# Kernel optimization log

Measured on AMD Instinct MI355X. Metric: run time of the kernel, lower is better.

The kernel has to match this reference:

```python
import jax, jax.numpy as jnp
import numpy as np
import math

N, S, C, K, V = 32, 4096, 1, 512, 128
TARGET_SCALE = 0.06  # normalize_scale == embedding_scale when normalize=True


def setup_inputs() -> dict:
    key = jax.random.key(0)
    k1, k2 = jax.random.split(key)
    x0 = jax.random.normal(k1, (N, S, C, V), dtype=jnp.float32)
    emb = jax.random.normal(k2, (C, K, V), dtype=jnp.float32) * TARGET_SCALE
    # after_update(): renormalize each code vector to norm = embedding_scale*sqrt(V)
    tn = TARGET_SCALE * math.sqrt(V)
    emb = emb * (tn / jnp.linalg.norm(emb, axis=2, keepdims=True))
    return {"x0": x0, "embedding0": emb}


def _vq_forward(x0, embedding0):
    tn = TARGET_SCALE * math.sqrt(V)
    # normalize inputs and codebook to the same norm (normalize=True path)
    x = tn * x0 / jnp.linalg.norm(x0, axis=3, keepdims=True)              # (N,S,C,V)
    emb = tn * embedding0 / jnp.linalg.norm(embedding0, axis=2, keepdims=True)  # (C,K,V)

    xf = x.reshape(N * S, C, V)
    x2 = jnp.sum(xf * xf, axis=2)                     # (NS, C)
    e2 = jnp.sum(emb * emb, axis=2)                   # (C, K)
    dots = jnp.einsum('ncv,ckv->nck', xf, emb)        # (NS, C, K)
    d2 = x2[:, :, None] + e2[None, :, :] - 2.0 * dots
    index = jnp.argmin(d2, axis=2)                    # (NS, C) int

    # entropy of code usage: histc over n_classes, normalized by len(index)=NS
    hist = jnp.zeros((K,), jnp.float32).at[index.reshape(-1)].add(1.0)
    prob = hist / float(N * S)
    entropy = -jnp.sum(jnp.where(hist > 0, prob * jnp.log(jnp.where(hist > 0, prob, 1.0)), 0.0))

    # gather selected code vectors per channel
    output = emb[jnp.arange(C)[None, :], index]       # (NS, C, V)
    output = output.reshape(x.shape)                  # (N,S,C,V)

    sg = jax.lax.stop_gradient
    out0 = sg(output - x) + x                                              # straight-through
    out1 = jnp.sum((sg(x) - output) ** 2, axis=3)                          # codebook loss (N,S,C)
    out2 = jnp.sum((x - sg(output)) ** 2, axis=3) + jnp.sum((x - x0) ** 2, axis=3)  # commitment + norm penalty
    return out0, out1, out2, entropy


def reference(x0, embedding0):
    return _vq_forward(x0, embedding0)
```

## Files before the change

kernel.cpp:

```cpp
#include <hip/hip_runtime.h>
#include <math.h>

#define VDIM   128
#define KCODES 512
#define NROWS  (32 * 4096)
#define TILE_ROWS 512
#define NBLK (NROWS / TILE_ROWS)
#define TN 0.67882250993908565f

typedef __attribute__((ext_vector_type(8))) short bf16x8;
typedef __attribute__((ext_vector_type(4))) float f32x4;

__device__ __forceinline__ unsigned short f2bf(float f) {
    unsigned u = __float_as_uint(f);
    unsigned r = u + 0x7FFFu + ((u >> 16) & 1u);
    return (unsigned short)(r >> 16);
}

__device__ __forceinline__ bf16x8 pack8(f32x4 a, f32x4 b) {
    bf16x8 v;
    v[0] = (short)f2bf(a[0]); v[1] = (short)f2bf(a[1]);
    v[2] = (short)f2bf(a[2]); v[3] = (short)f2bf(a[3]);
    v[4] = (short)f2bf(b[0]); v[5] = (short)f2bf(b[1]);
    v[6] = (short)f2bf(b[2]); v[7] = (short)f2bf(b[3]);
    return v;
}

__global__ __launch_bounds__(1024, 4) void vq_fused(
        const float* __restrict__ x0,
        const float* __restrict__ emb0,
        unsigned short* __restrict__ hist_part,
        float* __restrict__ out0,
        float* __restrict__ out1,
        float* __restrict__ out2) {
    __shared__ uint4 sB[8192];
    __shared__ float sscale[KCODES];
    __shared__ int   shist[KCODES];
    __shared__ int   sbesti[TILE_ROWS];
    __shared__ float sdot[TILE_ROWS];
    __shared__ float sn0[TILE_ROWS];

    int t = threadIdx.x;
    int w = t >> 6;
    int l = t & 63;
    int n15 = l & 15;
    int q = l >> 4;

    int rowbase = blockIdx.x * TILE_ROWS + (w << 5);
    f32x4 ax[2][4][2];
    #pragma unroll
    for (int s = 0; s < 2; ++s) {
        const float* xrow = x0 + (size_t)(rowbase + (s << 4) + n15) * VDIM + (q << 3);
        #pragma unroll
        for (int kc = 0; kc < 4; ++kc) {
            const f32x4* xp = (const f32x4*)(xrow + (kc << 5));
            ax[s][kc][0] = __builtin_nontemporal_load(xp);
            ax[s][kc][1] = __builtin_nontemporal_load(xp + 1);
        }
    }

    if (t < KCODES) shist[t] = 0;

    #pragma unroll 4
    for (int i = 0; i < 32; ++i) {
        int k = (w << 5) + i;
        const float* row = emb0 + (size_t)k * VDIM;
        float a = row[l];
        float b = row[l + 64];
        float ss = a * a + b * b;
        #pragma unroll
        for (int off = 32; off; off >>= 1) ss += __shfl_xor(ss, off);
        if (l == 0) sscale[k] = TN / sqrtf(ss);
    }
    __syncthreads();

    #pragma unroll
    for (int i = 0; i < 8; ++i) {
        int g = (i << 10) + t;
        int k = ((g >> 8) << 4) | (g & 15);
        int d0 = ((g >> 4) & 15) << 3;
        float s = sscale[k];
        const f32x4* ep = (const f32x4*)(emb0 + (size_t)k * VDIM + d0);
        f32x4 a = ep[0], b = ep[1];
        f32x4 as, bs;
        as[0] = a[0] * s; as[1] = a[1] * s; as[2] = a[2] * s; as[3] = a[3] * s;
        bs[0] = b[0] * s; bs[1] = b[1] * s; bs[2] = b[2] * s; bs[3] = b[3] * s;
        ((bf16x8*)sB)[g] = pack8(as, bs);
    }

    bf16x8 afr[2][4];
    float nsq[2];
    #pragma unroll
    for (int s = 0; s < 2; ++s) {
        float p0 = 0.f, p1 = 0.f;
        #pragma unroll
        for (int kc = 0; kc < 4; ++kc) {
            f32x4 a = ax[s][kc][0], b = ax[s][kc][1];
            p0 = fmaf(a[0], a[0], p0); p1 = fmaf(a[1], a[1], p1);
            p0 = fmaf(a[2], a[2], p0); p1 = fmaf(a[3], a[3], p1);
            p0 = fmaf(b[0], b[0], p0); p1 = fmaf(b[1], b[1], p1);
            p0 = fmaf(b[2], b[2], p0); p1 = fmaf(b[3], b[3], p1);
            afr[s][kc] = pack8(a, b);
        }
        nsq[s] = p0 + p1;
        nsq[s] += __shfl_xor(nsq[s], 16, 64);
        nsq[s] += __shfl_xor(nsq[s], 32, 64);
    }

    float best[2][4];
    int   bidx[2][4];
    #pragma unroll
    for (int s = 0; s < 2; ++s)
        #pragma unroll
        for (int r = 0; r < 4; ++r) { best[s][r] = -3.4e38f; bidx[s][r] = 0; }

    const f32x4 zero4 = {0.f, 0.f, 0.f, 0.f};

    __syncthreads();

    #pragma unroll 2
    for (int cn = 0; cn < 32; ++cn) {
        const bf16x8* bls = ((const bf16x8*)sB) + (cn << 8) + l;
        bf16x8 b0 = bls[0], b1 = bls[64], b2 = bls[128], b3 = bls[192];
        int nbase = (cn << 4) + n15;
        #pragma unroll
        for (int s = 0; s < 2; ++s) {
            f32x4 acc = __builtin_amdgcn_mfma_f32_16x16x32_bf16(afr[s][0], b0, zero4, 0, 0, 0);
            acc = __builtin_amdgcn_mfma_f32_16x16x32_bf16(afr[s][1], b1, acc, 0, 0, 0);
            acc = __builtin_amdgcn_mfma_f32_16x16x32_bf16(afr[s][2], b2, acc, 0, 0, 0);
            acc = __builtin_amdgcn_mfma_f32_16x16x32_bf16(afr[s][3], b3, acc, 0, 0, 0);
            #pragma unroll
            for (int r = 0; r < 4; ++r) {
                float d = acc[r];
                if (d > best[s][r]) { best[s][r] = d; bidx[s][r] = nbase; }
            }
        }
    }

    #pragma unroll
    for (int m = 1; m <= 8; m <<= 1) {
        #pragma unroll
        for (int s = 0; s < 2; ++s)
            #pragma unroll
            for (int r = 0; r < 4; ++r) {
                float ov = __shfl_xor(best[s][r], m, 64);
                int   oi = __shfl_xor(bidx[s][r], m, 64);
                if (ov > best[s][r] || (ov == best[s][r] && oi < bidx[s][r])) {
                    best[s][r] = ov; bidx[s][r] = oi;
                }
            }
    }

    if (n15 == 0) {
        #pragma unroll
        for (int s = 0; s < 2; ++s)
            #pragma unroll
            for (int r = 0; r < 4; ++r) {
                int lr = (w << 5) + (s << 4) + (q << 2) + r;
                sbesti[lr] = bidx[s][r];
                sdot[lr]   = best[s][r];
            }
    }
    if (q == 0) {
        #pragma unroll
        for (int s = 0; s < 2; ++s) sn0[(w << 5) + (s << 4) + n15] = nsq[s];
    }
    __syncthreads();

    size_t blockrow = (size_t)blockIdx.x * TILE_ROWS;
    #pragma unroll
    for (int pass = 0; pass < 16; ++pass) {
        int lr = (pass << 5) + (t >> 5);
        int v4 = t & 31;
        int bi = sbesti[lr];
        float s = sscale[bi];
        f32x4 e = *((const f32x4*)(emb0 + (size_t)bi * VDIM) + v4);
        f32x4 o;
        o[0] = e[0] * s; o[1] = e[1] * s; o[2] = e[2] * s; o[3] = e[3] * s;
        __builtin_nontemporal_store(o, (f32x4*)(out0 + (blockrow + lr) * (size_t)VDIM) + v4);
    }

    if (t < TILE_ROWS) {
        size_t row = blockrow + t;
        int bi = sbesti[t];
        float dotv = sdot[t];
        float nn = sn0[t];
        float sc = TN / sqrtf(nn);
        float o1 = 2.f * TN * TN - 2.f * sc * dotv;
        __builtin_nontemporal_store(o1, &out1[row]);
        float sm = sc - 1.f;
        __builtin_nontemporal_store(o1 + sm * sm * nn, &out2[row]);
        atomicAdd(&shist[bi], 1);
    }
    __syncthreads();

    if (t < KCODES)
        hist_part[((size_t)blockIdx.x << 9) + t] = (unsigned short)shist[t];
}

__global__ __launch_bounds__(1024) void entropy_k(
        const unsigned short* __restrict__ hp,
        float* __restrict__ out) {
    __shared__ int   s2[1024];
    __shared__ float red[8];
    int t = threadIdx.x;
    int c = t & 511;
    int half = t >> 9;
    int sum = 0;
    #pragma unroll 8
    for (int b = half * 128; b < half * 128 + 128; ++b)
        sum += hp[(b << 9) + c];
    s2[t] = sum;
    __syncthreads();
    if (t < 512) {
        float h = (float)(s2[t] + s2[t + 512]);
        float p = h / (float)NROWS;
        float term = (h > 0.f) ? p * logf(p) : 0.f;
        #pragma unroll
        for (int off = 32; off; off >>= 1) term += __shfl_xor(term, off);
        if ((t & 63) == 0) red[t >> 6] = term;
    }
    __syncthreads();
    if (t == 0) {
        float ssum = 0.f;
        #pragma unroll
        for (int i = 0; i < 8; i++) ssum += red[i];
        out[0] = -ssum;
    }
}

extern "C" void kernel_launch(void* const* d_in, const int* in_sizes, int n_in,
                              void* d_out, int out_size, void* d_ws, size_t ws_size,
                              hipStream_t stream) {
    const float* x0   = (const float*)d_in[0];
    const float* emb0 = (const float*)d_in[1];

    unsigned short* hist_part = (unsigned short*)d_ws;

    float* out  = (float*)d_out;
    float* out0 = out;
    float* out1 = out0 + (size_t)NROWS * VDIM;
    float* out2 = out1 + NROWS;
    float* oent = out2 + NROWS;

    vq_fused<<<NBLK, 1024, 0, stream>>>(x0, emb0, hist_part, out0, out1, out2);
    entropy_k<<<1, 1024, 0, stream>>>(hist_part, oent);
}
```

Baseline: 166.5 us.

## Replace LDS-staged epilogue with wave shuffles and relax launch bounds

Each wave now writes its own 32 rows. Argmin indices, best dot products and row norms move between lanes with __shfl instead of going through shared arrays, which removes three LDS buffers and one block-wide barrier before the epilogue. The launch-bounds minimum of blocks per CU drops from 4 to 1, giving the compiler a larger register budget; shared-memory use already limits the kernel to one block per CU. The x0 loads also switch from nontemporal to regular loads. The shuffle-based epilogue adds shuffle instructions and predicated lanes, and it changes the write pattern to per-wave row groups.

```diff
diff --git a/kernel.cpp b/kernel.cpp
--- a/kernel.cpp
+++ b/kernel.cpp
@@ -26,7 +26,7 @@
     return v;
 }
 
-__global__ __launch_bounds__(1024, 4) void vq_fused(
+__global__ __launch_bounds__(1024, 1) void vq_fused(
         const float* __restrict__ x0,
         const float* __restrict__ emb0,
         unsigned short* __restrict__ hist_part,
@@ -36,9 +36,6 @@
     __shared__ uint4 sB[8192];
     __shared__ float sscale[KCODES];
     __shared__ int   shist[KCODES];
-    __shared__ int   sbesti[TILE_ROWS];
-    __shared__ float sdot[TILE_ROWS];
-    __shared__ float sn0[TILE_ROWS];
 
     int t = threadIdx.x;
     int w = t >> 6;
@@ -54,8 +51,8 @@
         #pragma unroll
         for (int kc = 0; kc < 4; ++kc) {
             const f32x4* xp = (const f32x4*)(xrow + (kc << 5));
-            ax[s][kc][0] = __builtin_nontemporal_load(xp);
-            ax[s][kc][1] = __builtin_nontemporal_load(xp + 1);
+            ax[s][kc][0] = xp[0];
+            ax[s][kc][1] = xp[1];
         }
     }
 
@@ -151,47 +148,42 @@
             }
     }
 
-    if (n15 == 0) {
-        #pragma unroll
-        for (int s = 0; s < 2; ++s)
-            #pragma unroll
-            for (int r = 0; r < 4; ++r) {
-                int lr = (w << 5) + (s << 4) + (q << 2) + r;
-                sbesti[lr] = bidx[s][r];
-                sdot[lr]   = best[s][r];
-            }
-    }
-    if (q == 0) {
-        #pragma unroll
-        for (int s = 0; s < 2; ++s) sn0[(w << 5) + (s << 4) + n15] = nsq[s];
-    }
-    __syncthreads();
-
-    size_t blockrow = (size_t)blockIdx.x * TILE_ROWS;
-    #pragma unroll
-    for (int pass = 0; pass < 16; ++pass) {
-        int lr = (pass << 5) + (t >> 5);
-        int v4 = t & 31;
-        int bi = sbesti[lr];
+    size_t wrow = (size_t)rowbase;
+    #pragma unroll
+    for (int p = 0; p < 16; ++p) {
+        const int a0 = 2 * p, a1 = 2 * p + 1;
+        int biLo = __shfl(bidx[a0 >> 4][a0 & 3], ((a0 >> 2) & 3) << 4, 64);
+        int biHi = __shfl(bidx[a1 >> 4][a1 & 3], ((a1 >> 2) & 3) << 4, 64);
+        int bi = (l >= 32) ? biHi : biLo;
         float s = sscale[bi];
+        int v4 = l & 31;
+        size_t grow = wrow + (p << 1) + (l >> 5);
         f32x4 e = *((const f32x4*)(emb0 + (size_t)bi * VDIM) + v4);
         f32x4 o;
         o[0] = e[0] * s; o[1] = e[1] * s; o[2] = e[2] * s; o[3] = e[3] * s;
-        __builtin_nontemporal_store(o, (f32x4*)(out0 + (blockrow + lr) * (size_t)VDIM) + v4);
-    }
-
-    if (t < TILE_ROWS) {
-        size_t row = blockrow + t;
-        int bi = sbesti[t];
-        float dotv = sdot[t];
-        float nn = sn0[t];
-        float sc = TN / sqrtf(nn);
-        float o1 = 2.f * TN * TN - 2.f * sc * dotv;
-        __builtin_nontemporal_store(o1, &out1[row]);
-        float sm = sc - 1.f;
-        __builtin_nontemporal_store(o1 + sm * sm * nn, &out2[row]);
-        atomicAdd(&shist[bi], 1);
-    }
+        __builtin_nontemporal_store(o, (f32x4*)(out0 + grow * (size_t)VDIM) + v4);
+    }
+
+    #pragma unroll
+    for (int s = 0; s < 2; ++s)
+        #pragma unroll
+        for (int r = 0; r < 4; ++r) {
+            int src = (l & 12) << 2;
+            float dv = __shfl(best[s][r], src, 64);
+            int   bv = __shfl(bidx[s][r], src, 64);
+            float nn = __shfl(nsq[s], l & 15, 64);
+            bool act = (l < 32) && ((l >> 4) == s) && ((l & 3) == r);
+            if (act) {
+                size_t row = wrow + l;
+                float sc = TN / sqrtf(nn);
+                float o1 = 2.f * TN * TN - 2.f * sc * dv;
+                __builtin_nontemporal_store(o1, &out1[row]);
+                float sm = sc - 1.f;
+                __builtin_nontemporal_store(o1 + sm * sm * nn, &out2[row]);
+                atomicAdd(&shist[bv], 1);
+            }
+        }
+
     __syncthreads();
 
     if (t < KCODES)
```

Measured after the change: 158.9 us. 4.5% less time.
